# Kernel tuning notes

Hardware: AMD Instinct MI355X
Metric: run time of the kernel (lower is better)

The kernel has to match this reference:

```python
import jax, jax.numpy as jnp
import numpy as np

BS = 16  # block_size

def setup_inputs() -> dict:
    key = jax.random.key(0)
    k1, k2, k3, k4, k5 = jax.random.split(key, 5)
    B, C, H, W = 4, 192, 256, 256
    x = jax.random.normal(k1, (B, C, H, W), dtype=jnp.float32)
    s = 1.0 / np.sqrt(C)
    qkv_w = jax.random.normal(k2, (3 * C, C), dtype=jnp.float32) * s
    qkv_b = jax.random.normal(k3, (3 * C,), dtype=jnp.float32) * 0.01
    proj_w = jax.random.normal(k4, (C, C), dtype=jnp.float32) * s
    proj_b = jax.random.normal(k5, (C,), dtype=jnp.float32) * 0.01
    return {"x": x, "qkv_w": qkv_w, "qkv_b": qkv_b, "proj_w": proj_w, "proj_b": proj_b}

def reference(x, qkv_w, qkv_b, proj_w, proj_b):
    B, C, H, W = x.shape
    nh, nw = H // BS, W // BS
    N = BS * BS  # tokens per window
    # [B,C,H,W] -> [B*nh*nw, C, N]  (windowing, matches torch unfold/unfold)
    xb = x.reshape(B, C, nh, BS, nw, BS).transpose(0, 2, 4, 1, 3, 5)
    xb = xb.reshape(B * nh * nw, C, N)
    # 1x1-conv QKV projection as a GEMM over channels
    qkv = jnp.einsum('oc,bcn->bon', qkv_w, xb) + qkv_b[None, :, None]  # [Bb,3C,N]
    q, k, v = jnp.split(qkv, 3, axis=1)  # each [Bb, C, N]
    # attention: softmax(q^T k) over last dim (no scaling, as in original)
    att = jax.nn.softmax(jnp.einsum('bcn,bcm->bnm', q, k), axis=-1)  # [Bb,N,N]
    out = jnp.einsum('bnm,bcm->bcn', att, v)  # [Bb, C, N]
    # un-window back to [B, C, H, W]
    y = out.reshape(B, nh, nw, C, BS, BS).transpose(0, 3, 1, 4, 2, 5)
    y = y.reshape(B, C, H, W)
    # 1x1-conv output projection + residual
    proj = jnp.einsum('oc,bchw->bohw', proj_w, y) + proj_b[None, :, None, None]
    return proj + x
```

## Files before the change

kernel.cpp:

```cpp
#include <hip/hip_runtime.h>
#include <stdint.h>

typedef _Float16 f16;
typedef __attribute__((ext_vector_type(8))) _Float16 f16x8;
typedef __attribute__((ext_vector_type(4))) float f32x4;

#define MFMA(a, b, c) __builtin_amdgcn_mfma_f32_16x16x32_f16((a), (b), (c), 0, 0, 0)

static constexpr int C = 192;

union U8x { uint2 u2[2]; f16x8 v; };

__global__ void wconv_kernel(const float* __restrict__ qkv_w, const float* __restrict__ proj_w,
                             f16* __restrict__ wq, f16* __restrict__ wp) {
    int i = blockIdx.x * 256 + threadIdx.x;
    if (i < 576 * 192) wq[i] = (f16)qkv_w[i];
    if (i < 192 * 192) wp[i] = (f16)proj_w[i];
}

#define XS 200
__global__ __launch_bounds__(256, 4)
void qkv_kernel(const float* __restrict__ x, const f16* __restrict__ wq,
                const float* __restrict__ qkv_b,
                f16* __restrict__ Qp, f16* __restrict__ Kp, f16* __restrict__ vv) {
    __shared__ f16 xs[64 * XS];
    const int tid = threadIdx.x;
    const int wg = blockIdx.x;
    const int win = wg >> 2, tb = wg & 3;
    const int batch = win >> 8, wh = (win >> 4) & 15, ww = win & 15;
    const int i0 = tb * 4;

    for (int e = 0; e < 12; ++e) {
        int f = e * 1024 + tid * 4;
        int c = f >> 6, nl = f & 63;
        int i = nl >> 4, j = nl & 15;
        const float4 v4 = *(const float4*)(x + (((size_t)(batch * C + c) * 256 + (wh * 16 + i0 + i)) * 256 + ww * 16 + j));
        xs[(nl + 0) * XS + c] = (f16)v4.x;
        xs[(nl + 1) * XS + c] = (f16)v4.y;
        xs[(nl + 2) * XS + c] = (f16)v4.z;
        xs[(nl + 3) * XS + c] = (f16)v4.w;
    }
    __syncthreads();

    const int wave = tid >> 6, lane = tid & 63, l15 = lane & 15, qd = lane >> 4;
    for (int rb = wave; rb < 9; rb += 4) {
        f32x4 acc[4][4] = {};
#pragma unroll
        for (int k = 0; k < 6; ++k) {
            const int c0 = k * 32 + qd * 8;
            f16x8 af[4], bf[4];
#pragma unroll
            for (int mi = 0; mi < 4; ++mi)
                af[mi] = *(const f16x8*)(wq + (rb * 64 + mi * 16 + l15) * C + c0);
#pragma unroll
            for (int ti = 0; ti < 4; ++ti)
                bf[ti] = *(const f16x8*)(xs + (ti * 16 + l15) * XS + c0);
#pragma unroll
            for (int mi = 0; mi < 4; ++mi)
#pragma unroll
                for (int ti = 0; ti < 4; ++ti)
                    acc[mi][ti] = MFMA(af[mi], bf[ti], acc[mi][ti]);
        }
#pragma unroll
        for (int mi = 0; mi < 4; ++mi) {
            const int ob = rb * 64 + mi * 16 + qd * 4;
            const float b0 = qkv_b[ob + 0], b1 = qkv_b[ob + 1], b2 = qkv_b[ob + 2], b3 = qkv_b[ob + 3];
#pragma unroll
            for (int ti = 0; ti < 4; ++ti) {
                const int tok = tb * 64 + ti * 16 + l15;
                if (ob < 384) {
                    union { f16 h[4]; uint2 u; } pk;
                    pk.h[0] = (f16)(acc[mi][ti][0] + b0);
                    pk.h[1] = (f16)(acc[mi][ti][1] + b1);
                    pk.h[2] = (f16)(acc[mi][ti][2] + b2);
                    pk.h[3] = (f16)(acc[mi][ti][3] + b3);
                    const int c4 = (ob < 192) ? (ob >> 2) : ((ob - 192) >> 2);
                    f16* base = (ob < 192) ? Qp : Kp;
                    *(uint2*)(base + (((size_t)win * 48 + c4) * 256 + tok) * 4) = pk.u;
                } else {
                    const int c2 = ob - 384;
                    vv[((size_t)win * C + c2 + 0) * 256 + tok] = (f16)(acc[mi][ti][0] + b0);
                    vv[((size_t)win * C + c2 + 1) * 256 + tok] = (f16)(acc[mi][ti][1] + b1);
                    vv[((size_t)win * C + c2 + 2) * 256 + tok] = (f16)(acc[mi][ti][2] + b2);
                    vv[((size_t)win * C + c2 + 3) * 256 + tok] = (f16)(acc[mi][ti][3] + b3);
                }
            }
        }
    }
}

#define SQS 200
#define SPS 136
__global__ __launch_bounds__(256, 3)
void attn_kernel(const f16* __restrict__ Qp, const f16* __restrict__ Kp,
                 const f16* __restrict__ vv, const f16* __restrict__ wp,
                 const float* __restrict__ proj_b, const float* __restrict__ x,
                 float* __restrict__ out) {
    __shared__ f16 sQ[64 * SQS];
    __shared__ f16 sP[64 * SPS];
    __shared__ float sRed[4][64];
    __shared__ float sMax[64];
    __shared__ float sSum[64];

    const int tid = threadIdx.x;
    const int wg = blockIdx.x;
    const int win = ((wg >> 5) << 3) | (wg & 7);
    const int rblk = (wg >> 3) & 3;
    const int n0 = rblk * 64;
    const int batch = win >> 8, wh = (win >> 4) & 15, ww = win & 15;
    const int wave = tid >> 6, lane = tid & 63, l15 = lane & 15, qd = lane >> 4;

    for (int it = 0; it < 12; ++it) {
        int ch = it * 256 + tid;
        int n = ch & 63, c4 = ch >> 6;
        *(uint2*)(sQ + n * SQS + c4 * 4) =
            *(const uint2*)(Qp + (((size_t)win * 48 + c4) * 256 + n0 + n) * 4);
    }
    __syncthreads();

    f32x4 accS[4][4] = {};
#pragma unroll
    for (int k = 0; k < 6; ++k) {
        const int c0 = k * 32 + qd * 8;
        const int c4 = c0 >> 2;
        f16x8 af[4], bf[4];
#pragma unroll
        for (int mi = 0; mi < 4; ++mi)
            af[mi] = *(const f16x8*)(sQ + (mi * 16 + l15) * SQS + c0);
#pragma unroll
        for (int ti = 0; ti < 4; ++ti) {
            const int m = wave * 64 + ti * 16 + l15;
            const size_t a = (((size_t)win * 48 + c4) * 256 + m) * 4;
            U8x b;
            b.u2[0] = *(const uint2*)(Kp + a);
            b.u2[1] = *(const uint2*)(Kp + a + 1024);
            bf[ti] = b.v;
        }
#pragma unroll
        for (int mi = 0; mi < 4; ++mi)
#pragma unroll
            for (int ti = 0; ti < 4; ++ti)
                accS[mi][ti] = MFMA(af[mi], bf[ti], accS[mi][ti]);
    }

    float pm[4][4];
#pragma unroll
    for (int mi = 0; mi < 4; ++mi)
#pragma unroll
        for (int r = 0; r < 4; ++r) {
            float m = fmaxf(fmaxf(accS[mi][0][r], accS[mi][1][r]),
                            fmaxf(accS[mi][2][r], accS[mi][3][r]));
#pragma unroll
            for (int d = 1; d < 16; d <<= 1) m = fmaxf(m, __shfl_xor(m, d, 64));
            pm[mi][r] = m;
        }
    if (l15 == 0) {
#pragma unroll
        for (int mi = 0; mi < 4; ++mi)
#pragma unroll
            for (int r = 0; r < 4; ++r) sRed[wave][mi * 16 + qd * 4 + r] = pm[mi][r];
    }
    __syncthreads();
    if (tid < 64)
        sMax[tid] = fmaxf(fmaxf(sRed[0][tid], sRed[1][tid]), fmaxf(sRed[2][tid], sRed[3][tid]));
    __syncthreads();

    union PK { f16 h[4]; uint2 u; };
    PK pH[4][4];
    float ps[4][4];
#pragma unroll
    for (int mi = 0; mi < 4; ++mi)
#pragma unroll
        for (int r = 0; r < 4; ++r) {
            const float M = sMax[mi * 16 + qd * 4 + r];
            float s = 0.f;
#pragma unroll
            for (int ti = 0; ti < 4; ++ti) {
                float e = __expf(accS[mi][ti][r] - M);
                pH[mi][ti].h[r] = (f16)e;
                s += e;
            }
#pragma unroll
            for (int d = 1; d < 16; d <<= 1) s += __shfl_xor(s, d, 64);
            ps[mi][r] = s;
        }
    if (l15 == 0) {
#pragma unroll
        for (int mi = 0; mi < 4; ++mi)
#pragma unroll
            for (int r = 0; r < 4; ++r) sRed[wave][mi * 16 + qd * 4 + r] = ps[mi][r];
    }
    __syncthreads();
    if (tid < 64) sSum[tid] = sRed[0][tid] + sRed[1][tid] + sRed[2][tid] + sRed[3][tid];

    f32x4 accO[4][3] = {};
#pragma unroll
    for (int h = 0; h < 2; ++h) {
        if ((wave >> 1) == h) {
            const int cl = (wave & 1) * 64;
#pragma unroll
            for (int mi = 0; mi < 4; ++mi)
#pragma unroll
                for (int ti = 0; ti < 4; ++ti)
#pragma unroll
                    for (int r = 0; r < 4; ++r)
                        sP[(mi * 16 + qd * 4 + r) * SPS + cl + ti * 16 + l15] = pH[mi][ti].h[r];
        }
        __syncthreads();
#pragma unroll
        for (int k = 0; k < 4; ++k) {
            const int ml = k * 32 + qd * 8;
            const int m0 = h * 128 + ml;
            f16x8 af[4], bf[3];
#pragma unroll
            for (int tn = 0; tn < 4; ++tn)
                af[tn] = *(const f16x8*)(sP + (tn * 16 + l15) * SPS + ml);
#pragma unroll
            for (int tc = 0; tc < 3; ++tc)
                bf[tc] = *(const f16x8*)(vv + ((size_t)win * C + wave * 48 + tc * 16 + l15) * 256 + m0);
#pragma unroll
            for (int tn = 0; tn < 4; ++tn)
#pragma unroll
                for (int tc = 0; tc < 3; ++tc)
                    accO[tn][tc] = MFMA(af[tn], bf[tc], accO[tn][tc]);
        }
        if (h == 0) __syncthreads();
    }

    f16* sOT = sQ;
#pragma unroll
    for (int tn = 0; tn < 4; ++tn)
#pragma unroll
        for (int r = 0; r < 4; ++r) {
            const int n = tn * 16 + qd * 4 + r;
            const float rs = 1.0f / sSum[n];
#pragma unroll
            for (int tc = 0; tc < 3; ++tc)
                sOT[n * SQS + wave * 48 + tc * 16 + l15] = (f16)(accO[tn][tc][r] * rs);
        }
    __syncthreads();

    f32x4 accP[3][4] = {};
#pragma unroll
    for (int k = 0; k < 6; ++k) {
        const int c0 = k * 32 + qd * 8;
        f16x8 af[3], bf[4];
#pragma unroll
        for (int to = 0; to < 3; ++to)
            af[to] = *(const f16x8*)(wp + (wave * 48 + to * 16 + l15) * C + c0);
#pragma unroll
        for (int tn = 0; tn < 4; ++tn)
            bf[tn] = *(const f16x8*)(sOT + (tn * 16 + l15) * SQS + c0);
#pragma unroll
        for (int to = 0; to < 3; ++to)
#pragma unroll
            for (int tn = 0; tn < 4; ++tn)
                accP[to][tn] = MFMA(af[to], bf[tn], accP[to][tn]);
    }
#pragma unroll
    for (int to = 0; to < 3; ++to)
#pragma unroll
        for (int r = 0; r < 4; ++r) {
            const int o = wave * 48 + to * 16 + qd * 4 + r;
            const float pb = proj_b[o];
#pragma unroll
            for (int tn = 0; tn < 4; ++tn) {
                const size_t idx = (((size_t)(batch * C + o) * 256) + wh * 16 + rblk * 4 + tn) * 256 + ww * 16 + l15;
                out[idx] = accP[to][tn][r] + pb + x[idx];
            }
        }
}

extern "C" void kernel_launch(void* const* d_in, const int* in_sizes, int n_in,
                              void* d_out, int out_size, void* d_ws, size_t ws_size,
                              hipStream_t stream) {
    const float* x      = (const float*)d_in[0];
    const float* qkv_w  = (const float*)d_in[1];
    const float* qkv_b  = (const float*)d_in[2];
    const float* proj_w = (const float*)d_in[3];
    const float* proj_b = (const float*)d_in[4];
    float* out = (float*)d_out;

    char* ws = (char*)d_ws;
    const size_t QKV_BYTES = (size_t)1024 * 256 * 192 * 2;
    f16* Qp = (f16*)(ws);
    f16* Kp = (f16*)(ws + QKV_BYTES);
    f16* vv = (f16*)(ws + 2 * QKV_BYTES);
    f16* wq = (f16*)(ws + 3 * QKV_BYTES);
    f16* wp = (f16*)(ws + 3 * QKV_BYTES + 576 * 192 * 2);

    wconv_kernel<<<432, 256, 0, stream>>>(qkv_w, proj_w, wq, wp);
    qkv_kernel<<<4096, 256, 0, stream>>>(x, wq, qkv_b, Qp, Kp, vv);
    attn_kernel<<<4096, 256, 0, stream>>>(Qp, Kp, vv, wp, proj_b, x, out);
}
```

Measured before the change: 699.9 us.

## Fold QKV weights algebraically: compute x^T Wq^T Wk x and fold V into projection

Precomputes M = Wq^T Wk (plus a bias row), so scores become x^T (M x) + per-key bias, and folds Wv into the output projection (Wo = Wp Wv, with a combined bias). The first GEMM now produces only 193 channel rows instead of 576, and attention uses raw x (fp16) as the value operand. Query-side bias terms that are constant along the key axis are dropped because softmax cancels them. This reduces GEMM work and intermediate HBM traffic, but changes fp16 rounding because of the products of fused weights, and adds a small weight-prep GEMM kernel.

```diff
diff --git a/kernel.cpp b/kernel.cpp
--- a/kernel.cpp
+++ b/kernel.cpp
@@ -11,18 +11,45 @@
 
 union U8x { uint2 u2[2]; f16x8 v; };
 
-__global__ void wconv_kernel(const float* __restrict__ qkv_w, const float* __restrict__ proj_w,
-                             f16* __restrict__ wq, f16* __restrict__ wp) {
-    int i = blockIdx.x * 256 + threadIdx.x;
-    if (i < 576 * 192) wq[i] = (f16)qkv_w[i];
-    if (i < 192 * 192) wp[i] = (f16)proj_w[i];
+__global__ __launch_bounds__(256)
+void prep_kernel(const float* __restrict__ qkv_w, const float* __restrict__ qkv_b,
+                 const float* __restrict__ proj_w, const float* __restrict__ proj_b,
+                 f16* __restrict__ Mh, f16* __restrict__ Wo, float* __restrict__ b2) {
+    const int idx = blockIdx.x * 256 + threadIdx.x;
+    if (idx < 256 * 192) {
+        const int r = idx / 192, c = idx % 192;
+        float s = 0.f;
+        if (r < 192) {
+#pragma unroll 4
+            for (int o = 0; o < 192; ++o)
+                s += qkv_w[o * 192 + r] * qkv_w[(192 + o) * 192 + c];
+        } else if (r == 192) {
+#pragma unroll 4
+            for (int o = 0; o < 192; ++o)
+                s += qkv_b[o] * qkv_w[(192 + o) * 192 + c];
+        }
+        Mh[idx] = (f16)s;
+    } else if (idx < 256 * 192 + 192 * 192) {
+        const int j = idx - 256 * 192;
+        const int r = j / 192, c = j % 192;
+        float s = 0.f;
+#pragma unroll 4
+        for (int c2 = 0; c2 < 192; ++c2)
+            s += proj_w[r * 192 + c2] * qkv_w[(384 + c2) * 192 + c];
+        Wo[j] = (f16)s;
+    } else if (idx < 256 * 192 + 192 * 192 + 192) {
+        const int o = idx - (256 * 192 + 192 * 192);
+        float s = proj_b[o];
+        for (int c2 = 0; c2 < 192; ++c2)
+            s += proj_w[o * 192 + c2] * qkv_b[384 + c2];
+        b2[o] = s;
+    }
 }
 
 #define XS 200
 __global__ __launch_bounds__(256, 4)
-void qkv_kernel(const float* __restrict__ x, const f16* __restrict__ wq,
-                const float* __restrict__ qkv_b,
-                f16* __restrict__ Qp, f16* __restrict__ Kp, f16* __restrict__ vv) {
+void xt_kernel(const float* __restrict__ x, const f16* __restrict__ Mh,
+               f16* __restrict__ tpk, f16* __restrict__ xh) {
     __shared__ f16 xs[64 * XS];
     const int tid = threadIdx.x;
     const int wg = blockIdx.x;
@@ -43,59 +70,62 @@
     __syncthreads();
 
     const int wave = tid >> 6, lane = tid & 63, l15 = lane & 15, qd = lane >> 4;
-    for (int rb = wave; rb < 9; rb += 4) {
-        f32x4 acc[4][4] = {};
-#pragma unroll
-        for (int k = 0; k < 6; ++k) {
-            const int c0 = k * 32 + qd * 8;
-            f16x8 af[4], bf[4];
-#pragma unroll
-            for (int mi = 0; mi < 4; ++mi)
-                af[mi] = *(const f16x8*)(wq + (rb * 64 + mi * 16 + l15) * C + c0);
-#pragma unroll
-            for (int ti = 0; ti < 4; ++ti)
-                bf[ti] = *(const f16x8*)(xs + (ti * 16 + l15) * XS + c0);
-#pragma unroll
-            for (int mi = 0; mi < 4; ++mi)
+    const int rb = wave;
+    const int nmi = (wave == 3) ? 1 : 4;
+    f32x4 acc[4][4] = {};
+#pragma unroll
+    for (int k = 0; k < 6; ++k) {
+        const int c0 = k * 32 + qd * 8;
+        f16x8 af[4], bf[4];
+#pragma unroll
+        for (int mi = 0; mi < 4; ++mi)
+            if (mi < nmi)
+                af[mi] = *(const f16x8*)(Mh + (rb * 64 + mi * 16 + l15) * C + c0);
+#pragma unroll
+        for (int ti = 0; ti < 4; ++ti)
+            bf[ti] = *(const f16x8*)(xs + (ti * 16 + l15) * XS + c0);
+#pragma unroll
+        for (int mi = 0; mi < 4; ++mi)
+            if (mi < nmi)
 #pragma unroll
                 for (int ti = 0; ti < 4; ++ti)
                     acc[mi][ti] = MFMA(af[mi], bf[ti], acc[mi][ti]);
-        }
-#pragma unroll
-        for (int mi = 0; mi < 4; ++mi) {
-            const int ob = rb * 64 + mi * 16 + qd * 4;
-            const float b0 = qkv_b[ob + 0], b1 = qkv_b[ob + 1], b2 = qkv_b[ob + 2], b3 = qkv_b[ob + 3];
+    }
+#pragma unroll
+    for (int mi = 0; mi < 4; ++mi) {
+        if (mi >= nmi) continue;
+        const int c4 = rb * 16 + mi * 4 + qd;
+        if (c4 < 49) {
 #pragma unroll
             for (int ti = 0; ti < 4; ++ti) {
                 const int tok = tb * 64 + ti * 16 + l15;
-                if (ob < 384) {
-                    union { f16 h[4]; uint2 u; } pk;
-                    pk.h[0] = (f16)(acc[mi][ti][0] + b0);
-                    pk.h[1] = (f16)(acc[mi][ti][1] + b1);
-                    pk.h[2] = (f16)(acc[mi][ti][2] + b2);
-                    pk.h[3] = (f16)(acc[mi][ti][3] + b3);
-                    const int c4 = (ob < 192) ? (ob >> 2) : ((ob - 192) >> 2);
-                    f16* base = (ob < 192) ? Qp : Kp;
-                    *(uint2*)(base + (((size_t)win * 48 + c4) * 256 + tok) * 4) = pk.u;
-                } else {
-                    const int c2 = ob - 384;
-                    vv[((size_t)win * C + c2 + 0) * 256 + tok] = (f16)(acc[mi][ti][0] + b0);
-                    vv[((size_t)win * C + c2 + 1) * 256 + tok] = (f16)(acc[mi][ti][1] + b1);
-                    vv[((size_t)win * C + c2 + 2) * 256 + tok] = (f16)(acc[mi][ti][2] + b2);
-                    vv[((size_t)win * C + c2 + 3) * 256 + tok] = (f16)(acc[mi][ti][3] + b3);
-                }
+                union { f16 h[4]; uint2 u; } pk;
+                pk.h[0] = (f16)acc[mi][ti][0];
+                pk.h[1] = (f16)acc[mi][ti][1];
+                pk.h[2] = (f16)acc[mi][ti][2];
+                pk.h[3] = (f16)acc[mi][ti][3];
+                *(uint2*)(tpk + (((size_t)win * 49 + c4) * 256 + tok) * 4) = pk.u;
             }
         }
     }
+    for (int it = 0; it < 12; ++it) {
+        int e = it * 256 + tid;
+        int c = e >> 4, t4 = (e & 15) * 4;
+        union { f16 h[4]; uint2 u; } pk;
+        pk.h[0] = xs[(t4 + 0) * XS + c];
+        pk.h[1] = xs[(t4 + 1) * XS + c];
+        pk.h[2] = xs[(t4 + 2) * XS + c];
+        pk.h[3] = xs[(t4 + 3) * XS + c];
+        *(uint2*)(xh + ((size_t)win * C + c) * 256 + tb * 64 + t4) = pk.u;
+    }
 }
 
 #define SQS 200
-#define SPS 136
-__global__ __launch_bounds__(256, 3)
-void attn_kernel(const f16* __restrict__ Qp, const f16* __restrict__ Kp,
-                 const f16* __restrict__ vv, const f16* __restrict__ wp,
-                 const float* __restrict__ proj_b, const float* __restrict__ x,
-                 float* __restrict__ out) {
+#define SPS 72
+__global__ __launch_bounds__(256, 4)
+void attn_kernel(const float* __restrict__ x, const f16* __restrict__ tpk,
+                 const f16* __restrict__ xh, const f16* __restrict__ Wo,
+                 const float* __restrict__ b2, float* __restrict__ out) {
     __shared__ f16 sQ[64 * SQS];
     __shared__ f16 sP[64 * SPS];
     __shared__ float sRed[4][64];
@@ -106,16 +136,23 @@
     const int wg = blockIdx.x;
     const int win = ((wg >> 5) << 3) | (wg & 7);
     const int rblk = (wg >> 3) & 3;
-    const int n0 = rblk * 64;
     const int batch = win >> 8, wh = (win >> 4) & 15, ww = win & 15;
     const int wave = tid >> 6, lane = tid & 63, l15 = lane & 15, qd = lane >> 4;
 
-    for (int it = 0; it < 12; ++it) {
-        int ch = it * 256 + tid;
-        int n = ch & 63, c4 = ch >> 6;
-        *(uint2*)(sQ + n * SQS + c4 * 4) =
-            *(const uint2*)(Qp + (((size_t)win * 48 + c4) * 256 + n0 + n) * 4);
-    }
+    for (int e = 0; e < 12; ++e) {
+        int f = e * 1024 + tid * 4;
+        int c = f >> 6, nl = f & 63;
+        int i = nl >> 4, j = nl & 15;
+        const float4 v4 = *(const float4*)(x + (((size_t)(batch * C + c) * 256 + (wh * 16 + rblk * 4 + i)) * 256 + ww * 16 + j));
+        sQ[(nl + 0) * SQS + c] = (f16)v4.x;
+        sQ[(nl + 1) * SQS + c] = (f16)v4.y;
+        sQ[(nl + 2) * SQS + c] = (f16)v4.z;
+        sQ[(nl + 3) * SQS + c] = (f16)v4.w;
+    }
+    float vm[4];
+#pragma unroll
+    for (int ti = 0; ti < 4; ++ti)
+        vm[ti] = (float)tpk[(((size_t)win * 49 + 48) * 256 + wave * 64 + ti * 16 + l15) * 4];
     __syncthreads();
 
     f32x4 accS[4][4] = {};
@@ -130,10 +167,10 @@
 #pragma unroll
         for (int ti = 0; ti < 4; ++ti) {
             const int m = wave * 64 + ti * 16 + l15;
-            const size_t a = (((size_t)win * 48 + c4) * 256 + m) * 4;
+            const size_t a = (((size_t)win * 49 + c4) * 256 + m) * 4;
             U8x b;
-            b.u2[0] = *(const uint2*)(Kp + a);
-            b.u2[1] = *(const uint2*)(Kp + a + 1024);
+            b.u2[0] = *(const uint2*)(tpk + a);
+            b.u2[1] = *(const uint2*)(tpk + a + 1024);
             bf[ti] = b.v;
         }
 #pragma unroll
@@ -142,6 +179,13 @@
             for (int ti = 0; ti < 4; ++ti)
                 accS[mi][ti] = MFMA(af[mi], bf[ti], accS[mi][ti]);
     }
+#pragma unroll
+    for (int mi = 0; mi < 4; ++mi)
+#pragma unroll
+        for (int ti = 0; ti < 4; ++ti)
+#pragma unroll
+            for (int r = 0; r < 4; ++r)
+                accS[mi][ti][r] += vm[ti];
 
     float pm[4][4];
 #pragma unroll
@@ -195,36 +239,35 @@
 
     f32x4 accO[4][3] = {};
 #pragma unroll
-    for (int h = 0; h < 2; ++h) {
-        if ((wave >> 1) == h) {
-            const int cl = (wave & 1) * 64;
+    for (int h = 0; h < 4; ++h) {
+        if (wave == h) {
 #pragma unroll
             for (int mi = 0; mi < 4; ++mi)
 #pragma unroll
                 for (int ti = 0; ti < 4; ++ti)
 #pragma unroll
                     for (int r = 0; r < 4; ++r)
-                        sP[(mi * 16 + qd * 4 + r) * SPS + cl + ti * 16 + l15] = pH[mi][ti].h[r];
+                        sP[(mi * 16 + qd * 4 + r) * SPS + ti * 16 + l15] = pH[mi][ti].h[r];
         }
         __syncthreads();
 #pragma unroll
-        for (int k = 0; k < 4; ++k) {
+        for (int k = 0; k < 2; ++k) {
             const int ml = k * 32 + qd * 8;
-            const int m0 = h * 128 + ml;
+            const int m0 = h * 64 + ml;
             f16x8 af[4], bf[3];
 #pragma unroll
             for (int tn = 0; tn < 4; ++tn)
                 af[tn] = *(const f16x8*)(sP + (tn * 16 + l15) * SPS + ml);
 #pragma unroll
             for (int tc = 0; tc < 3; ++tc)
-                bf[tc] = *(const f16x8*)(vv + ((size_t)win * C + wave * 48 + tc * 16 + l15) * 256 + m0);
+                bf[tc] = *(const f16x8*)(xh + ((size_t)win * C + wave * 48 + tc * 16 + l15) * 256 + m0);
 #pragma unroll
             for (int tn = 0; tn < 4; ++tn)
 #pragma unroll
                 for (int tc = 0; tc < 3; ++tc)
                     accO[tn][tc] = MFMA(af[tn], bf[tc], accO[tn][tc]);
         }
-        if (h == 0) __syncthreads();
+        if (h < 3) __syncthreads();
     }
 
     f16* sOT = sQ;
@@ -247,7 +290,7 @@
         f16x8 af[3], bf[4];
 #pragma unroll
         for (int to = 0; to < 3; ++to)
-            af[to] = *(const f16x8*)(wp + (wave * 48 + to * 16 + l15) * C + c0);
+            af[to] = *(const f16x8*)(Wo + (wave * 48 + to * 16 + l15) * C + c0);
 #pragma unroll
         for (int tn = 0; tn < 4; ++tn)
             bf[tn] = *(const f16x8*)(sOT + (tn * 16 + l15) * SQS + c0);
@@ -262,7 +305,7 @@
 #pragma unroll
         for (int r = 0; r < 4; ++r) {
             const int o = wave * 48 + to * 16 + qd * 4 + r;
-            const float pb = proj_b[o];
+            const float pb = b2[o];
 #pragma unroll
             for (int tn = 0; tn < 4; ++tn) {
                 const size_t idx = (((size_t)(batch * C + o) * 256) + wh * 16 + rblk * 4 + tn) * 256 + ww * 16 + l15;
@@ -282,14 +325,17 @@
     float* out = (float*)d_out;
 
     char* ws = (char*)d_ws;
-    const size_t QKV_BYTES = (size_t)1024 * 256 * 192 * 2;
-    f16* Qp = (f16*)(ws);
-    f16* Kp = (f16*)(ws + QKV_BYTES);
-    f16* vv = (f16*)(ws + 2 * QKV_BYTES);
-    f16* wq = (f16*)(ws + 3 * QKV_BYTES);
-    f16* wp = (f16*)(ws + 3 * QKV_BYTES + 576 * 192 * 2);
-
-    wconv_kernel<<<432, 256, 0, stream>>>(qkv_w, proj_w, wq, wp);
-    qkv_kernel<<<4096, 256, 0, stream>>>(x, wq, qkv_b, Qp, Kp, vv);
-    attn_kernel<<<4096, 256, 0, stream>>>(Qp, Kp, vv, wp, proj_b, x, out);
+    const size_t TPK_BYTES = (size_t)1024 * 49 * 256 * 4 * 2;
+    const size_t XH_BYTES  = (size_t)1024 * 192 * 256 * 2;
+    const size_t MH_BYTES  = (size_t)256 * 192 * 2;
+    const size_t WO_BYTES  = (size_t)192 * 192 * 2;
+    f16*   tpk = (f16*)(ws);
+    f16*   xh  = (f16*)(ws + TPK_BYTES);
+    f16*   Mh  = (f16*)(ws + TPK_BYTES + XH_BYTES);
+    f16*   Wo  = (f16*)(ws + TPK_BYTES + XH_BYTES + MH_BYTES);
+    float* b2  = (float*)(ws + TPK_BYTES + XH_BYTES + MH_BYTES + WO_BYTES);
+
+    prep_kernel<<<337, 256, 0, stream>>>(qkv_w, qkv_b, proj_w, proj_b, Mh, Wo, b2);
+    xt_kernel<<<4096, 256, 0, stream>>>(x, Mh, tpk, xh);
+    attn_kernel<<<4096, 256, 0, stream>>>(x, tpk, xh, Wo, b2, out);
 }
```

New measurement: 790.6 us. 13.0% more time.
